# Kernel tuning notes

Measured on AMD Instinct MI355X. Metric: run time of the kernel, lower is better.

Reference implementation:

```python
import jax, jax.numpy as jnp
import numpy as np

N_NODES = 50000
N_EDGES = 800000
T = 3          # number of graph snapshots
L = 2          # num_layers
D = 128        # node feat dim == hidden dim
DE = 16        # edge feat dim


def setup_inputs() -> dict:
    key = jax.random.key(0)
    ks = jax.random.split(key, 12)
    return {
        "src": jax.random.randint(ks[0], (T, N_EDGES), 0, N_NODES, dtype=jnp.int32),
        "dst": jax.random.randint(ks[1], (T, N_EDGES), 0, N_NODES, dtype=jnp.int32),
        "n_feats": jax.random.normal(ks[2], (T, N_NODES, D), dtype=jnp.float32),
        "e_feats": jax.random.normal(ks[3], (T, N_EDGES, DE), dtype=jnp.float32),
        "W0": jax.random.normal(ks[4], (L, D, D), dtype=jnp.float32) * (1.0 / np.sqrt(D)),
        "lstm_Wih": jax.random.normal(ks[5], (L, 4 * D, D), dtype=jnp.float32) * (1.0 / np.sqrt(D)),
        "lstm_Whh": jax.random.normal(ks[6], (L, 4 * D, D), dtype=jnp.float32) * (1.0 / np.sqrt(D)),
        "lstm_bih": jnp.zeros((L, 4 * D), dtype=jnp.float32),
        "lstm_bhh": jnp.zeros((L, 4 * D), dtype=jnp.float32),
        "a_w": jax.random.normal(ks[7], (L, 2 * D + DE), dtype=jnp.float32) * 0.05,
    }


def _lstm(x, Wih, Whh, bih, bhh):
    # x: [S, H] unbatched sequence (S = D rows of W). PyTorch gate order i,f,g,o.
    H = Whh.shape[1]
    b = bih + bhh

    def step(carry, xt):
        h, c = carry
        gates = Wih @ xt + Whh @ h + b          # [4H]
        i = jax.nn.sigmoid(gates[:H])
        f = jax.nn.sigmoid(gates[H:2 * H])
        g = jnp.tanh(gates[2 * H:3 * H])
        o = jax.nn.sigmoid(gates[3 * H:])
        c = f * c + i * g
        h = o * jnp.tanh(c)
        return (h, c), h

    init = (jnp.zeros((H,), x.dtype), jnp.zeros((H,), x.dtype))
    _, hs = jax.lax.scan(step, init, x)
    return hs  # [S, H]


def _gat(src, dst, nf, ef, W, a_w, n_nodes):
    D_ = nf.shape[1]
    a_src, a_edge, a_dst = a_w[:D_], a_w[D_:D_ + ef.shape[1]], a_w[D_ + ef.shape[1]:]
    ft = nf @ W                                  # [N, H]
    s_src = nf @ a_src                           # [N]
    s_dst = nf @ a_dst                           # [N]
    score = s_src[src] + ef @ a_edge + s_dst[dst]  # [E]
    # edge softmax over destination neighborhoods
    mx = jax.ops.segment_max(score, dst, num_segments=n_nodes)
    ex = jnp.exp(score - mx[dst])
    den = jax.ops.segment_sum(ex, dst, num_segments=n_nodes)
    den = jnp.where(den == 0, 1.0, den)
    alpha = ex / den[dst]                        # [E]
    out = jax.ops.segment_sum(ft[src] * alpha[:, None], dst, num_segments=n_nodes)
    return jax.nn.leaky_relu(out)                # [N, H]


def reference(src, dst, n_feats, e_feats, W0, lstm_Wih, lstm_Whh, lstm_bih, lstm_bhh, a_w):
    n_nodes = n_feats.shape[1]
    feats = [n_feats[j] for j in range(n_feats.shape[0])]
    for i in range(W0.shape[0]):
        W = W0[i]
        for j in range(len(feats)):
            W = _lstm(W, lstm_Wih[i], lstm_Whh[i], lstm_bih[i], lstm_bhh[i])
            feats[j] = _gat(src[j], dst[j], feats[j], e_feats[j], W, a_w[i], n_nodes)
    return feats[-1]
```

## Files before the change

kernel.cpp:

```cpp
#include <hip/hip_runtime.h>
#include <cstdint>
#include <cstddef>

#define N_NODES 50000
#define N_EDGES 800000
#define D 128
#define DE 16
#define NBLK 196

typedef float v2f __attribute__((ext_vector_type(2)));

__global__ void csr_hist(const int* __restrict__ dst, int* __restrict__ count){
  int e = blockIdx.x*256 + threadIdx.x;
  if (e < N_EDGES) atomicAdd(&count[dst[e]], 1);
}

__global__ __launch_bounds__(256) void csr_blocksum(const int* __restrict__ count,
                                                    int* __restrict__ bsum){
  __shared__ int red[4];
  int i = blockIdx.x*256 + threadIdx.x;
  int v = (i < N_NODES) ? count[i] : 0;
  #pragma unroll
  for (int off=32; off; off>>=1) v += __shfl_down(v, off);
  if ((threadIdx.x & 63) == 0) red[threadIdx.x>>6] = v;
  __syncthreads();
  if (threadIdx.x == 0) bsum[blockIdx.x] = red[0]+red[1]+red[2]+red[3];
}

__global__ __launch_bounds__(256) void csr_scan_bsum(const int* __restrict__ bsum,
                                                     int* __restrict__ boff){
  __shared__ int s[256];
  int t = threadIdx.x;
  int v = (t < NBLK) ? bsum[t] : 0;
  s[t] = v; __syncthreads();
  for (int off=1; off<256; off<<=1){
    int u = (t >= off) ? s[t-off] : 0;
    __syncthreads(); s[t] += u; __syncthreads();
  }
  if (t < NBLK) boff[t] = s[t] - v;
}

__global__ __launch_bounds__(256) void csr_downsweep(const int* __restrict__ count,
    const int* __restrict__ boff, int* __restrict__ row_start, int* __restrict__ cursor){
  __shared__ int s[256];
  int t = threadIdx.x;
  int i = blockIdx.x*256 + t;
  int v = (i < N_NODES) ? count[i] : 0;
  s[t] = v; __syncthreads();
  for (int off=1; off<256; off<<=1){
    int u = (t >= off) ? s[t-off] : 0;
    __syncthreads(); s[t] += u; __syncthreads();
  }
  int excl = boff[blockIdx.x] + s[t] - v;
  if (i <= N_NODES) row_start[i] = excl;
  if (i <  N_NODES) cursor[i]   = excl;
}

__global__ void csr_scatter(const int* __restrict__ src, const int* __restrict__ dst,
                            int* __restrict__ cursor, int* __restrict__ perm,
                            int* __restrict__ src_perm){
  int e = blockIdx.x*256 + threadIdx.x;
  if (e >= N_EDGES) return;
  int d = dst[e];
  int pos = atomicAdd(&cursor[d], 1);
  perm[pos] = e;
  src_perm[pos] = src[e];
}

__global__ __launch_bounds__(512) void lstm_pre(const float* __restrict__ Wih,
     const float* __restrict__ bih, const float* __restrict__ bhh,
     const float* __restrict__ xin, float* __restrict__ P){
  __shared__ float xs[128];
  int i = blockIdx.x >> 7, t = blockIdx.x & 127;
  const float* x = xin + (size_t)i*16384;
  if (threadIdx.x < 128) xs[threadIdx.x] = x[t*128 + threadIdx.x];
  __syncthreads();
  int r = threadIdx.x;
  const float4* wr = (const float4*)(Wih + (size_t)(i*512 + r)*128);
  const float4* x4 = (const float4*)xs;
  float acc = bih[i*512+r] + bhh[i*512+r];
  #pragma unroll
  for (int k=0;k<32;k++){
    float4 w = wr[k]; float4 xv = x4[k];
    acc += w.x*xv.x + w.y*xv.y + w.z*xv.z + w.w*xv.w;
  }
  P[(size_t)(i*128+t)*512 + r] = acc;
}

__global__ __launch_bounds__(512, 2) void lstm_scan(const float* __restrict__ Whh,
     const float* __restrict__ P, float* __restrict__ xout){
  __shared__ float hs[128];
  __shared__ float part[4][512];
  const int i  = blockIdx.x;
  const int r  = threadIdx.x;
  const int w  = r >> 6;
  const int l  = r & 63;
  const int kc = w >> 1;
  const int rh = w & 1;
  const int row0 = rh*256 + l*4;
  v2f wv[4][16];
  {
    const float* base = Whh + (size_t)i*512*128 + (size_t)row0*128 + kc*32;
    #pragma unroll
    for (int ri=0; ri<4; ri++){
      const v2f* p2 = (const v2f*)(base + ri*128);
      #pragma unroll
      for (int j=0;j<16;j++) wv[ri][j] = p2[j];
    }
  }
  float c = 0.f;
  float hreg = 0.f;
  if (r < 128) hs[r] = 0.f;
  __syncthreads();
  const float* Pi = P + (size_t)i*128*512;
  float* xo = xout + (size_t)i*128*128;
  for (int t=0; t<128; t++){
    float p0=0.f, p1=0.f, p2=0.f, p3=0.f;
    if (r < 128){
      p0 = Pi[t*512 +   0 + r];
      p1 = Pi[t*512 + 128 + r];
      p2 = Pi[t*512 + 256 + r];
      p3 = Pi[t*512 + 384 + r];
    }
    float4 hbuf[8];
    {
      const float4* h4 = ((const float4*)hs) + kc*8;
      #pragma unroll
      for (int j=0;j<8;j++) hbuf[j] = h4[j];
    }
    const v2f* h2 = (const v2f*)hbuf;
    v2f a0 = (v2f)(0.f), a1 = (v2f)(0.f), a2 = (v2f)(0.f), a3 = (v2f)(0.f);
    #pragma unroll
    for (int j=0;j<16;j++){
      v2f hv = h2[j];
      a0 = __builtin_elementwise_fma(wv[0][j], hv, a0);
      a1 = __builtin_elementwise_fma(wv[1][j], hv, a1);
      a2 = __builtin_elementwise_fma(wv[2][j], hv, a2);
      a3 = __builtin_elementwise_fma(wv[3][j], hv, a3);
    }
    float4 pr;
    pr.x = a0.x + a0.y;
    pr.y = a1.x + a1.y;
    pr.z = a2.x + a2.y;
    pr.w = a3.x + a3.y;
    *(float4*)&part[kc][row0] = pr;
    __syncthreads();
    if (r < 128){
      int j = r;
      float s0 = ((part[0][      j] + part[1][      j]) + (part[2][      j] + part[3][      j])) + p0;
      float s1 = ((part[0][128 + j] + part[1][128 + j]) + (part[2][128 + j] + part[3][128 + j])) + p1;
      float s2 = ((part[0][256 + j] + part[1][256 + j]) + (part[2][256 + j] + part[3][256 + j])) + p2;
      float s3 = ((part[0][384 + j] + part[1][384 + j]) + (part[2][384 + j] + part[3][384 + j])) + p3;
      float gi = __builtin_amdgcn_rcpf(1.f + __expf(-s0));
      float gf = __builtin_amdgcn_rcpf(1.f + __expf(-s1));
      float xg = fminf(fmaxf(s2, -15.f), 15.f);
      float eg = __expf(2.f*xg);
      float gg = (eg - 1.f) * __builtin_amdgcn_rcpf(eg + 1.f);
      float go = __builtin_amdgcn_rcpf(1.f + __expf(-s3));
      c = gf*c + gi*gg;
      float xc = fminf(fmaxf(c, -15.f), 15.f);
      float e2 = __expf(2.f*xc);
      float th = (e2 - 1.f) * __builtin_amdgcn_rcpf(e2 + 1.f);
      hreg = go*th;
      hs[j] = hreg;
    }
    __syncthreads();
    if (r < 128) xo[t*128 + r] = hreg;
  }
}

__global__ __launch_bounds__(256) void gat_transform(const float* __restrict__ f,
    const float* __restrict__ W, const float* __restrict__ aw,
    float* __restrict__ ft, float* __restrict__ s_src){
  __shared__ float Ws[64*128];
  __shared__ float fs[128*36];
  int n0 = blockIdx.x * 32;
  {
    int n = threadIdx.x >> 3, kq = threadIdx.x & 7;
    int gn = n0 + n;
    #pragma unroll
    for (int p=0;p<4;p++){
      int k = kq*16 + p*4;
      float4 v = make_float4(0.f,0.f,0.f,0.f);
      if (gn < N_NODES) v = *(const float4*)(f + (size_t)gn*128 + k);
      fs[(k+0)*36+n] = v.x; fs[(k+1)*36+n] = v.y;
      fs[(k+2)*36+n] = v.z; fs[(k+3)*36+n] = v.w;
    }
  }
  int jg = threadIdx.x & 31, ng = threadIdx.x >> 5;
  v2f A00=(v2f)(0.f), A01=A00, A10=A00, A11=A00;
  v2f A20=A00, A21=A00, A30=A00, A31=A00;
  for (int kk=0; kk<128; kk+=64){
    __syncthreads();
    {
      const float4* W4 = (const float4*)(W + (size_t)kk*128);
      float4* Ws4w = (float4*)Ws;
      for (int idx = threadIdx.x; idx < 2048; idx += 256) Ws4w[idx] = W4[idx];
    }
    __syncthreads();
    const float4* Ws4 = (const float4*)Ws;
    #pragma unroll 4
    for (int k2=0;k2<64;k2++){
      float4 wvv = Ws4[k2*32 + jg];
      v2f wl; wl.x = wvv.x; wl.y = wvv.y;
      v2f wh; wh.x = wvv.z; wh.y = wvv.w;
      float4 fv = *(const float4*)&fs[(kk+k2)*36 + (ng<<2)];
      v2f f0 = (v2f)(fv.x), f1 = (v2f)(fv.y), f2 = (v2f)(fv.z), f3 = (v2f)(fv.w);
      A00 = __builtin_elementwise_fma(wl, f0, A00);
      A01 = __builtin_elementwise_fma(wh, f0, A01);
      A10 = __builtin_elementwise_fma(wl, f1, A10);
      A11 = __builtin_elementwise_fma(wh, f1, A11);
      A20 = __builtin_elementwise_fma(wl, f2, A20);
      A21 = __builtin_elementwise_fma(wh, f2, A21);
      A30 = __builtin_elementwise_fma(wl, f3, A30);
      A31 = __builtin_elementwise_fma(wh, f3, A31);
    }
  }
  int nb = n0 + (ng<<2);
  float4 o0; o0.x=A00.x; o0.y=A00.y; o0.z=A01.x; o0.w=A01.y;
  float4 o1; o1.x=A10.x; o1.y=A10.y; o1.z=A11.x; o1.w=A11.y;
  float4 o2; o2.x=A20.x; o2.y=A20.y; o2.z=A21.x; o2.w=A21.y;
  float4 o3; o3.x=A30.x; o3.y=A30.y; o3.z=A31.x; o3.w=A31.y;
  if (nb+0 < N_NODES) *(float4*)(ft + (size_t)(nb+0)*128 + (jg<<2)) = o0;
  if (nb+1 < N_NODES) *(float4*)(ft + (size_t)(nb+1)*128 + (jg<<2)) = o1;
  if (nb+2 < N_NODES) *(float4*)(ft + (size_t)(nb+2)*128 + (jg<<2)) = o2;
  if (nb+3 < N_NODES) *(float4*)(ft + (size_t)(nb+3)*128 + (jg<<2)) = o3;
  if (threadIdx.x < 32){
    int gn = n0 + threadIdx.x;
    if (gn < N_NODES){
      float s = 0.f;
      for (int k=0;k<128;k++) s += fs[k*36 + threadIdx.x] * aw[k];
      s_src[gn] = s;
    }
  }
}

__global__ __launch_bounds__(256) void gat_edge_score(const int* __restrict__ perm,
    const int* __restrict__ src_perm, const float* __restrict__ s_src,
    const float* __restrict__ ef, const float* __restrict__ aw,
    float* __restrict__ score){
  int p = blockIdx.x*256 + threadIdx.x;
  if (p >= N_EDGES) return;
  int e = perm[p];
  int s = src_perm[p];
  const float4* A = (const float4*)(aw + 128);
  float4 A0=A[0], A1=A[1], A2=A[2], A3=A[3];
  const float4* ev = (const float4*)(ef + (size_t)e*16);
  float4 v0=ev[0], v1=ev[1], v2=ev[2], v3=ev[3];
  float acc = s_src[s];
  acc += v0.x*A0.x + v0.y*A0.y + v0.z*A0.z + v0.w*A0.w;
  acc += v1.x*A1.x + v1.y*A1.y + v1.z*A1.z + v1.w*A1.w;
  acc += v2.x*A2.x + v2.y*A2.y + v2.z*A2.z + v2.w*A2.w;
  acc += v3.x*A3.x + v3.y*A3.y + v3.z*A3.z + v3.w*A3.w;
  score[p] = acc;
}

__global__ __launch_bounds__(256) void gat_aggregate(const int* __restrict__ row_start,
    const int* __restrict__ src_perm, float* __restrict__ score,
    const float* __restrict__ ft, float* __restrict__ out){
  int lane = threadIdx.x & 63;
  int wv = threadIdx.x >> 6;
  int n = blockIdx.x*4 + wv;
  if (n >= N_NODES) return;
  int s = row_start[n], e = row_start[n+1];
  float m = -1e30f;
  for (int p = s+lane; p < e; p += 64) m = fmaxf(m, score[p]);
  #pragma unroll
  for (int off=32; off; off>>=1) m = fmaxf(m, __shfl_xor(m, off));
  float den = 0.f;
  for (int p = s+lane; p < e; p += 64){
    float ex = __expf(score[p]-m);
    den += ex;
    score[p] = ex;
  }
  #pragma unroll
  for (int off=32; off; off>>=1) den += __shfl_xor(den, off);
  float inv = (den > 0.f) ? 1.f/den : 0.f;
  float a0 = 0.f, a1 = 0.f;
  for (int p = s; p < e; p++){
    float al = score[p]*inv;
    int sp = src_perm[p];
    float2 v = ((const float2*)(ft + (size_t)sp*128))[lane];
    a0 += al*v.x; a1 += al*v.y;
  }
  float2 o;
  o.x = (a0 > 0.f) ? a0 : 0.01f*a0;
  o.y = (a1 > 0.f) ? a1 : 0.01f*a1;
  ((float2*)(out + (size_t)n*128))[lane] = o;
}

extern "C" void kernel_launch(void* const* d_in, const int* in_sizes, int n_in,
                              void* d_out, int out_size, void* d_ws, size_t ws_size,
                              hipStream_t stream){
  (void)in_sizes; (void)n_in; (void)out_size; (void)ws_size;
  const int*   src     = (const int*)d_in[0] + (size_t)2*N_EDGES;
  const int*   dst     = (const int*)d_in[1] + (size_t)2*N_EDGES;
  const float* n_feats = (const float*)d_in[2] + (size_t)2*N_NODES*D;
  const float* e_feats = (const float*)d_in[3] + (size_t)2*N_EDGES*DE;
  const float* W0      = (const float*)d_in[4];
  const float* Wih     = (const float*)d_in[5];
  const float* Whh     = (const float*)d_in[6];
  const float* bih     = (const float*)d_in[7];
  const float* bhh     = (const float*)d_in[8];
  const float* a_w     = (const float*)d_in[9];
  float* out = (float*)d_out;

  char* wsp = (char*)d_ws;
  auto alloc = [&](size_t bytes)->char*{
    char* p = wsp; wsp += (bytes + 255) & ~(size_t)255; return p;
  };
  float* P         = (float*)alloc((size_t)2*128*512*4);
  float* xA        = (float*)alloc((size_t)2*128*128*4);
  float* xB        = (float*)alloc((size_t)2*128*128*4);
  int*   count     = (int*)  alloc((size_t)N_NODES*4);
  int*   bsum      = (int*)  alloc((size_t)NBLK*4);
  int*   boff      = (int*)  alloc((size_t)NBLK*4);
  int*   row_start = (int*)  alloc((size_t)(N_NODES+1)*4);
  int*   cursor    = (int*)  alloc((size_t)N_NODES*4);
  int*   perm      = (int*)  alloc((size_t)N_EDGES*4);
  int*   src_perm  = (int*)  alloc((size_t)N_EDGES*4);
  float* score     = (float*)alloc((size_t)N_EDGES*4);
  float* s_src     = (float*)alloc((size_t)N_NODES*4);
  float* ft        = (float*)alloc((size_t)N_NODES*D*4);
  float* f1        = (float*)alloc((size_t)N_NODES*D*4);

  hipMemsetAsync(count, 0, (size_t)N_NODES*4, stream);
  csr_hist     <<<(N_EDGES+255)/256, 256, 0, stream>>>(dst, count);
  csr_blocksum <<<NBLK, 256, 0, stream>>>(count, bsum);
  csr_scan_bsum<<<1,    256, 0, stream>>>(bsum, boff);
  csr_downsweep<<<NBLK, 256, 0, stream>>>(count, boff, row_start, cursor);
  csr_scatter  <<<(N_EDGES+255)/256, 256, 0, stream>>>(src, dst, cursor, perm, src_perm);

  const float* xi = W0;
  float* xo = xA;
  for (int app=0; app<3; app++){
    lstm_pre <<<256, 512, 0, stream>>>(Wih, bih, bhh, xi, P);
    lstm_scan<<<2,   512, 0, stream>>>(Whh, P, xo);
    xi = xo;
    xo = (app==0) ? xB : xA;
  }
  const float* Wfin = xA;

  const float* fin = n_feats;
  for (int l=0; l<2; l++){
    float* outl = (l==0) ? f1 : out;
    gat_transform <<<(N_NODES+31)/32, 256, 0, stream>>>(fin, Wfin + (size_t)l*16384,
                                                        a_w + (size_t)l*272, ft, s_src);
    gat_edge_score<<<(N_EDGES+255)/256, 256, 0, stream>>>(perm, src_perm, s_src,
                                                          e_feats, a_w + (size_t)l*272, score);
    gat_aggregate <<<N_NODES/4, 256, 0, stream>>>(row_start, src_perm, score, ft, outl);
    fin = f1;
  }
}
```

Measured before the change: 930.5 us.

## Fuse three chained LSTM scans into one wavefront-pipelined kernel

Replaces the three sequential lstm_pre + lstm_scan launches with one precompute launch and a single fused kernel. That kernel runs the three LSTM applications as a diagonal wavefront: at step d, stage a processes timestep d-a, and stages 2 and 3 compute their input projection on the fly from the previous stage's hidden state using register-resident Wih. This removes two of the three serial 128-step latency chains and four kernel launches. In exchange it doubles register use for weights (launch bounds drop to 1 block per SM) and adds extra FMA work and shared-memory traffic to each step.

Result: slower. 1.841 ms (+97.8%).

```diff
diff --git a/kernel.cpp b/kernel.cpp
--- a/kernel.cpp
+++ b/kernel.cpp
@@ -87,10 +87,13 @@
   P[(size_t)(i*128+t)*512 + r] = acc;
 }
 
-__global__ __launch_bounds__(512, 2) void lstm_scan(const float* __restrict__ Whh,
-     const float* __restrict__ P, float* __restrict__ xout){
-  __shared__ float hs[128];
-  __shared__ float part[4][512];
+__global__ __launch_bounds__(512, 1) void lstm_fused(
+    const float* __restrict__ Whh, const float* __restrict__ Wih,
+    const float* __restrict__ bih, const float* __restrict__ bhh,
+    const float* __restrict__ P0, float* __restrict__ xout){
+  __shared__ float hs[3][128];
+  __shared__ float partW[3][4][512];
+  __shared__ float partP[2][4][512];
   const int i  = blockIdx.x;
   const int r  = threadIdx.x;
   const int w  = r >> 6;
@@ -98,59 +101,101 @@
   const int kc = w >> 1;
   const int rh = w & 1;
   const int row0 = rh*256 + l*4;
-  v2f wv[4][16];
+  v2f whh[4][16], wih[4][16];
   {
-    const float* base = Whh + (size_t)i*512*128 + (size_t)row0*128 + kc*32;
+    const float* bh = Whh + (size_t)i*65536 + (size_t)row0*128 + kc*32;
+    const float* bw = Wih + (size_t)i*65536 + (size_t)row0*128 + kc*32;
     #pragma unroll
     for (int ri=0; ri<4; ri++){
-      const v2f* p2 = (const v2f*)(base + ri*128);
+      const v2f* ph = (const v2f*)(bh + ri*128);
+      const v2f* pw = (const v2f*)(bw + ri*128);
       #pragma unroll
-      for (int j=0;j<16;j++) wv[ri][j] = p2[j];
-    }
+      for (int j=0;j<16;j++){ whh[ri][j] = ph[j]; wih[ri][j] = pw[j]; }
+    }
+  }
+  const int sa = r >> 7;
+  const int sj = r & 127;
+  float b0=0.f,b1=0.f,b2=0.f,b3=0.f;
+  if (sa==1 || sa==2){
+    b0 = bih[i*512 +       sj] + bhh[i*512 +       sj];
+    b1 = bih[i*512 + 128 + sj] + bhh[i*512 + 128 + sj];
+    b2 = bih[i*512 + 256 + sj] + bhh[i*512 + 256 + sj];
+    b3 = bih[i*512 + 384 + sj] + bhh[i*512 + 384 + sj];
   }
   float c = 0.f;
   float hreg = 0.f;
-  if (r < 128) hs[r] = 0.f;
+  if (r < 384) ((float*)hs)[r] = 0.f;
   __syncthreads();
-  const float* Pi = P + (size_t)i*128*512;
+  const float* Pi = P0 + (size_t)i*128*512;
   float* xo = xout + (size_t)i*128*128;
-  for (int t=0; t<128; t++){
-    float p0=0.f, p1=0.f, p2=0.f, p3=0.f;
-    if (r < 128){
-      p0 = Pi[t*512 +   0 + r];
-      p1 = Pi[t*512 + 128 + r];
-      p2 = Pi[t*512 + 256 + r];
-      p3 = Pi[t*512 + 384 + r];
-    }
-    float4 hbuf[8];
-    {
-      const float4* h4 = ((const float4*)hs) + kc*8;
-      #pragma unroll
-      for (int j=0;j<8;j++) hbuf[j] = h4[j];
-    }
-    const v2f* h2 = (const v2f*)hbuf;
-    v2f a0 = (v2f)(0.f), a1 = (v2f)(0.f), a2 = (v2f)(0.f), a3 = (v2f)(0.f);
+  for (int d=0; d<130; d++){
+    float pc0=0.f,pc1=0.f,pc2=0.f,pc3=0.f;
+    if (sa==0 && d<128){
+      pc0 = Pi[d*512 +       sj];
+      pc1 = Pi[d*512 + 128 + sj];
+      pc2 = Pi[d*512 + 256 + sj];
+      pc3 = Pi[d*512 + 384 + sj];
+    }
     #pragma unroll
-    for (int j=0;j<16;j++){
-      v2f hv = h2[j];
-      a0 = __builtin_elementwise_fma(wv[0][j], hv, a0);
-      a1 = __builtin_elementwise_fma(wv[1][j], hv, a1);
-      a2 = __builtin_elementwise_fma(wv[2][j], hv, a2);
-      a3 = __builtin_elementwise_fma(wv[3][j], hv, a3);
-    }
-    float4 pr;
-    pr.x = a0.x + a0.y;
-    pr.y = a1.x + a1.y;
-    pr.z = a2.x + a2.y;
-    pr.w = a3.x + a3.y;
-    *(float4*)&part[kc][row0] = pr;
+    for (int a=0; a<3; a++){
+      const int ta = d - a;
+      const bool rec  = (ta >= 0) && (ta < 128);
+      const bool feed = (a < 2) && (ta >= 1) && (ta <= 128);
+      if (rec || feed){
+        float4 hb[8];
+        const float4* h4 = ((const float4*)hs[a]) + kc*8;
+        #pragma unroll
+        for (int j=0;j<8;j++) hb[j] = h4[j];
+        const v2f* h2 = (const v2f*)hb;
+        if (rec){
+          v2f a0=(v2f)(0.f), a1=a0, a2=a0, a3=a0;
+          #pragma unroll
+          for (int j=0;j<16;j++){
+            v2f hv = h2[j];
+            a0 = __builtin_elementwise_fma(whh[0][j], hv, a0);
+            a1 = __builtin_elementwise_fma(whh[1][j], hv, a1);
+            a2 = __builtin_elementwise_fma(whh[2][j], hv, a2);
+            a3 = __builtin_elementwise_fma(whh[3][j], hv, a3);
+          }
+          float4 pr;
+          pr.x = a0.x + a0.y; pr.y = a1.x + a1.y;
+          pr.z = a2.x + a2.y; pr.w = a3.x + a3.y;
+          *(float4*)&partW[a][kc][row0] = pr;
+        }
+        if (feed){
+          v2f a0=(v2f)(0.f), a1=a0, a2=a0, a3=a0;
+          #pragma unroll
+          for (int j=0;j<16;j++){
+            v2f hv = h2[j];
+            a0 = __builtin_elementwise_fma(wih[0][j], hv, a0);
+            a1 = __builtin_elementwise_fma(wih[1][j], hv, a1);
+            a2 = __builtin_elementwise_fma(wih[2][j], hv, a2);
+            a3 = __builtin_elementwise_fma(wih[3][j], hv, a3);
+          }
+          float4 pr;
+          pr.x = a0.x + a0.y; pr.y = a1.x + a1.y;
+          pr.z = a2.x + a2.y; pr.w = a3.x + a3.y;
+          *(float4*)&partP[a][kc][row0] = pr;
+        }
+      }
+    }
     __syncthreads();
-    if (r < 128){
-      int j = r;
-      float s0 = ((part[0][      j] + part[1][      j]) + (part[2][      j] + part[3][      j])) + p0;
-      float s1 = ((part[0][128 + j] + part[1][128 + j]) + (part[2][128 + j] + part[3][128 + j])) + p1;
-      float s2 = ((part[0][256 + j] + part[1][256 + j]) + (part[2][256 + j] + part[3][256 + j])) + p2;
-      float s3 = ((part[0][384 + j] + part[1][384 + j]) + (part[2][384 + j] + part[3][384 + j])) + p3;
+    const int ts = d - sa;
+    if (sa < 3 && ts >= 0 && ts < 128){
+      const int j0 = sj, j1 = 128+sj, j2 = 256+sj, j3 = 384+sj;
+      float s0 = (partW[sa][0][j0]+partW[sa][1][j0])+(partW[sa][2][j0]+partW[sa][3][j0]);
+      float s1 = (partW[sa][0][j1]+partW[sa][1][j1])+(partW[sa][2][j1]+partW[sa][3][j1]);
+      float s2 = (partW[sa][0][j2]+partW[sa][1][j2])+(partW[sa][2][j2]+partW[sa][3][j2]);
+      float s3 = (partW[sa][0][j3]+partW[sa][1][j3])+(partW[sa][2][j3]+partW[sa][3][j3]);
+      if (sa == 0){
+        s0 += pc0; s1 += pc1; s2 += pc2; s3 += pc3;
+      } else {
+        const float (*pp)[512] = partP[sa-1];
+        s0 += ((pp[0][j0]+pp[1][j0])+(pp[2][j0]+pp[3][j0])) + b0;
+        s1 += ((pp[0][j1]+pp[1][j1])+(pp[2][j1]+pp[3][j1])) + b1;
+        s2 += ((pp[0][j2]+pp[1][j2])+(pp[2][j2]+pp[3][j2])) + b2;
+        s3 += ((pp[0][j3]+pp[1][j3])+(pp[2][j3]+pp[3][j3])) + b3;
+      }
       float gi = __builtin_amdgcn_rcpf(1.f + __expf(-s0));
       float gf = __builtin_amdgcn_rcpf(1.f + __expf(-s1));
       float xg = fminf(fmaxf(s2, -15.f), 15.f);
@@ -162,10 +207,10 @@
       float e2 = __expf(2.f*xc);
       float th = (e2 - 1.f) * __builtin_amdgcn_rcpf(e2 + 1.f);
       hreg = go*th;
-      hs[j] = hreg;
+      hs[sa][sj] = hreg;
     }
     __syncthreads();
-    if (r < 128) xo[t*128 + r] = hreg;
+    if (sa == 2 && ts >= 0 && ts < 128) xo[ts*128 + sj] = hreg;
   }
 }
 
@@ -310,8 +355,7 @@
     char* p = wsp; wsp += (bytes + 255) & ~(size_t)255; return p;
   };
   float* P         = (float*)alloc((size_t)2*128*512*4);
-  float* xA        = (float*)alloc((size_t)2*128*128*4);
-  float* xB        = (float*)alloc((size_t)2*128*128*4);
+  float* Wfin      = (float*)alloc((size_t)2*128*128*4);
   int*   count     = (int*)  alloc((size_t)N_NODES*4);
   int*   bsum      = (int*)  alloc((size_t)NBLK*4);
   int*   boff      = (int*)  alloc((size_t)NBLK*4);
@@ -331,15 +375,8 @@
   csr_downsweep<<<NBLK, 256, 0, stream>>>(count, boff, row_start, cursor);
   csr_scatter  <<<(N_EDGES+255)/256, 256, 0, stream>>>(src, dst, cursor, perm, src_perm);
 
-  const float* xi = W0;
-  float* xo = xA;
-  for (int app=0; app<3; app++){
-    lstm_pre <<<256, 512, 0, stream>>>(Wih, bih, bhh, xi, P);
-    lstm_scan<<<2,   512, 0, stream>>>(Whh, P, xo);
-    xi = xo;
-    xo = (app==0) ? xB : xA;
-  }
-  const float* Wfin = xA;
+  lstm_pre  <<<256, 512, 0, stream>>>(Wih, bih, bhh, W0, P);
+  lstm_fused<<<2,   512, 0, stream>>>(Whh, Wih, bih, bhh, P, Wfin);
 
   const float* fin = n_feats;
   for (int l=0; l<2; l++){
```

## Co-schedule CSR build and edge-score precompute inside LSTM scan kernels

Applied to the files above, without the earlier changes.

The separate CSR-construction kernels are folded into the LSTM pre/scan launches as extra blocks, so the serial 2-block LSTM scan overlaps with the histogram, prefix sums and scatter. The edge-feature dot products for both layers are computed once in unpermuted order alongside the first scan. The edge-score kernel then only gathers precomputed values. This removes launches and idle GPU time during the latency-bound scan. In exchange it adds an 800K x 2 float buffer and a random gather via perm.

New measurement: 838.3 us. 9.9% less time.

```diff
diff --git a/kernel.cpp b/kernel.cpp
--- a/kernel.cpp
+++ b/kernel.cpp
@@ -6,72 +6,17 @@
 #define N_EDGES 800000
 #define D 128
 #define DE 16
-#define NBLK 196
+#define HB 1563
+#define NB512 98
 
 typedef float v2f __attribute__((ext_vector_type(2)));
 
-__global__ void csr_hist(const int* __restrict__ dst, int* __restrict__ count){
-  int e = blockIdx.x*256 + threadIdx.x;
-  if (e < N_EDGES) atomicAdd(&count[dst[e]], 1);
-}
-
-__global__ __launch_bounds__(256) void csr_blocksum(const int* __restrict__ count,
-                                                    int* __restrict__ bsum){
-  __shared__ int red[4];
-  int i = blockIdx.x*256 + threadIdx.x;
-  int v = (i < N_NODES) ? count[i] : 0;
-  #pragma unroll
-  for (int off=32; off; off>>=1) v += __shfl_down(v, off);
-  if ((threadIdx.x & 63) == 0) red[threadIdx.x>>6] = v;
-  __syncthreads();
-  if (threadIdx.x == 0) bsum[blockIdx.x] = red[0]+red[1]+red[2]+red[3];
-}
-
-__global__ __launch_bounds__(256) void csr_scan_bsum(const int* __restrict__ bsum,
-                                                     int* __restrict__ boff){
-  __shared__ int s[256];
-  int t = threadIdx.x;
-  int v = (t < NBLK) ? bsum[t] : 0;
-  s[t] = v; __syncthreads();
-  for (int off=1; off<256; off<<=1){
-    int u = (t >= off) ? s[t-off] : 0;
-    __syncthreads(); s[t] += u; __syncthreads();
-  }
-  if (t < NBLK) boff[t] = s[t] - v;
-}
-
-__global__ __launch_bounds__(256) void csr_downsweep(const int* __restrict__ count,
-    const int* __restrict__ boff, int* __restrict__ row_start, int* __restrict__ cursor){
-  __shared__ int s[256];
-  int t = threadIdx.x;
-  int i = blockIdx.x*256 + t;
-  int v = (i < N_NODES) ? count[i] : 0;
-  s[t] = v; __syncthreads();
-  for (int off=1; off<256; off<<=1){
-    int u = (t >= off) ? s[t-off] : 0;
-    __syncthreads(); s[t] += u; __syncthreads();
-  }
-  int excl = boff[blockIdx.x] + s[t] - v;
-  if (i <= N_NODES) row_start[i] = excl;
-  if (i <  N_NODES) cursor[i]   = excl;
-}
-
-__global__ void csr_scatter(const int* __restrict__ src, const int* __restrict__ dst,
-                            int* __restrict__ cursor, int* __restrict__ perm,
-                            int* __restrict__ src_perm){
-  int e = blockIdx.x*256 + threadIdx.x;
-  if (e >= N_EDGES) return;
-  int d = dst[e];
-  int pos = atomicAdd(&cursor[d], 1);
-  perm[pos] = e;
-  src_perm[pos] = src[e];
-}
-
-__global__ __launch_bounds__(512) void lstm_pre(const float* __restrict__ Wih,
+
+__device__ void lstm_pre_body(const float* __restrict__ Wih,
      const float* __restrict__ bih, const float* __restrict__ bhh,
-     const float* __restrict__ xin, float* __restrict__ P){
+     const float* __restrict__ xin, float* __restrict__ P, int bid){
   __shared__ float xs[128];
-  int i = blockIdx.x >> 7, t = blockIdx.x & 127;
+  int i = bid >> 7, t = bid & 127;
   const float* x = xin + (size_t)i*16384;
   if (threadIdx.x < 128) xs[threadIdx.x] = x[t*128 + threadIdx.x];
   __syncthreads();
@@ -87,11 +32,10 @@
   P[(size_t)(i*128+t)*512 + r] = acc;
 }
 
-__global__ __launch_bounds__(512, 2) void lstm_scan(const float* __restrict__ Whh,
-     const float* __restrict__ P, float* __restrict__ xout){
+__device__ void lstm_scan_body(const float* __restrict__ Whh,
+     const float* __restrict__ P, float* __restrict__ xout, int i){
   __shared__ float hs[128];
   __shared__ float part[4][512];
-  const int i  = blockIdx.x;
   const int r  = threadIdx.x;
   const int w  = r >> 6;
   const int l  = r & 63;
@@ -169,6 +113,131 @@
   }
 }
 
+__device__ void csr_blocksum512(const int* __restrict__ count,
+                                int* __restrict__ bsum, int b){
+  __shared__ int red[8];
+  int t = threadIdx.x;
+  int i = b*512 + t;
+  int v = (i < N_NODES) ? count[i] : 0;
+  #pragma unroll
+  for (int off=32; off; off>>=1) v += __shfl_down(v, off);
+  if ((t & 63) == 0) red[t>>6] = v;
+  __syncthreads();
+  if (t == 0){
+    int s = 0;
+    #pragma unroll
+    for (int k=0;k<8;k++) s += red[k];
+    bsum[b] = s;
+  }
+}
+
+__device__ void csr_scan_bsum512(const int* __restrict__ bsum,
+                                 int* __restrict__ boff){
+  __shared__ int s[512];
+  int t = threadIdx.x;
+  int v = (t < NB512) ? bsum[t] : 0;
+  s[t] = v; __syncthreads();
+  for (int off=1; off<512; off<<=1){
+    int u = (t >= off) ? s[t-off] : 0;
+    __syncthreads(); s[t] += u; __syncthreads();
+  }
+  if (t < NB512) boff[t] = s[t] - v;
+}
+
+__device__ void csr_downsweep512(const int* __restrict__ count,
+    const int* __restrict__ boff, int* __restrict__ row_start,
+    int* __restrict__ cursor, int b){
+  __shared__ int s[512];
+  int t = threadIdx.x;
+  int i = b*512 + t;
+  int v = (i < N_NODES) ? count[i] : 0;
+  s[t] = v; __syncthreads();
+  for (int off=1; off<512; off<<=1){
+    int u = (t >= off) ? s[t-off] : 0;
+    __syncthreads(); s[t] += u; __syncthreads();
+  }
+  int excl = boff[b] + s[t] - v;
+  if (i <= N_NODES) row_start[i] = excl;
+  if (i <  N_NODES) cursor[i]   = excl;
+}
+
+__global__ __launch_bounds__(512) void k_pre(const float* __restrict__ Wih,
+     const float* __restrict__ bih, const float* __restrict__ bhh,
+     const float* __restrict__ xin, float* __restrict__ P){
+  lstm_pre_body(Wih, bih, bhh, xin, P, blockIdx.x);
+}
+
+__global__ __launch_bounds__(512, 2) void k_scan_hist_epart(
+    const float* __restrict__ Whh, const float* __restrict__ P,
+    float* __restrict__ xout, const int* __restrict__ dst,
+    int* __restrict__ count, const float* __restrict__ ef,
+    const float* __restrict__ aw, float* __restrict__ epart){
+  int b = blockIdx.x;
+  if (b < 2){ lstm_scan_body(Whh, P, xout, b); return; }
+  b -= 2;
+  if (b < HB){
+    int e = b*512 + threadIdx.x;
+    if (e < N_EDGES) atomicAdd(&count[dst[e]], 1);
+    return;
+  }
+  b -= HB;
+  int e = b*512 + threadIdx.x;
+  if (e < N_EDGES){
+    const float4* ev = (const float4*)(ef + (size_t)e*16);
+    float4 v0=ev[0], v1=ev[1], v2=ev[2], v3=ev[3];
+    #pragma unroll
+    for (int l=0; l<2; l++){
+      const float4* A = (const float4*)(aw + l*272 + 128);
+      float4 A0=A[0], A1=A[1], A2=A[2], A3=A[3];
+      float acc = v0.x*A0.x + v0.y*A0.y + v0.z*A0.z + v0.w*A0.w;
+      acc      += v1.x*A1.x + v1.y*A1.y + v1.z*A1.z + v1.w*A1.w;
+      acc      += v2.x*A2.x + v2.y*A2.y + v2.z*A2.z + v2.w*A2.w;
+      acc      += v3.x*A3.x + v3.y*A3.y + v3.z*A3.z + v3.w*A3.w;
+      epart[(size_t)l*N_EDGES + e] = acc;
+    }
+  }
+}
+
+__global__ __launch_bounds__(512) void k_pre_blocksum(const float* __restrict__ Wih,
+     const float* __restrict__ bih, const float* __restrict__ bhh,
+     const float* __restrict__ xin, float* __restrict__ P,
+     const int* __restrict__ count, int* __restrict__ bsum){
+  if (blockIdx.x < 256) lstm_pre_body(Wih, bih, bhh, xin, P, blockIdx.x);
+  else                  csr_blocksum512(count, bsum, blockIdx.x - 256);
+}
+
+__global__ __launch_bounds__(512, 2) void k_scan_scanbsum(
+    const float* __restrict__ Whh, const float* __restrict__ P,
+    float* __restrict__ xout, const int* __restrict__ bsum,
+    int* __restrict__ boff){
+  if (blockIdx.x < 2) lstm_scan_body(Whh, P, xout, blockIdx.x);
+  else                csr_scan_bsum512(bsum, boff);
+}
+
+__global__ __launch_bounds__(512) void k_pre_downsweep(const float* __restrict__ Wih,
+     const float* __restrict__ bih, const float* __restrict__ bhh,
+     const float* __restrict__ xin, float* __restrict__ P,
+     const int* __restrict__ count, const int* __restrict__ boff,
+     int* __restrict__ row_start, int* __restrict__ cursor){
+  if (blockIdx.x < 256) lstm_pre_body(Wih, bih, bhh, xin, P, blockIdx.x);
+  else                  csr_downsweep512(count, boff, row_start, cursor, blockIdx.x - 256);
+}
+
+__global__ __launch_bounds__(512, 2) void k_scan_scatter(
+    const float* __restrict__ Whh, const float* __restrict__ P,
+    float* __restrict__ xout, const int* __restrict__ src,
+    const int* __restrict__ dst, int* __restrict__ cursor,
+    int* __restrict__ perm, int* __restrict__ src_perm){
+  int b = blockIdx.x;
+  if (b < 2){ lstm_scan_body(Whh, P, xout, b); return; }
+  int e = (b-2)*512 + threadIdx.x;
+  if (e >= N_EDGES) return;
+  int d = dst[e];
+  int pos = atomicAdd(&cursor[d], 1);
+  perm[pos] = e;
+  src_perm[pos] = src[e];
+}
+
 __global__ __launch_bounds__(256) void gat_transform(const float* __restrict__ f,
     const float* __restrict__ W, const float* __restrict__ aw,
     float* __restrict__ ft, float* __restrict__ s_src){
@@ -237,22 +306,10 @@
 
 __global__ __launch_bounds__(256) void gat_edge_score(const int* __restrict__ perm,
     const int* __restrict__ src_perm, const float* __restrict__ s_src,
-    const float* __restrict__ ef, const float* __restrict__ aw,
-    float* __restrict__ score){
+    const float* __restrict__ epart_l, float* __restrict__ score){
   int p = blockIdx.x*256 + threadIdx.x;
   if (p >= N_EDGES) return;
-  int e = perm[p];
-  int s = src_perm[p];
-  const float4* A = (const float4*)(aw + 128);
-  float4 A0=A[0], A1=A[1], A2=A[2], A3=A[3];
-  const float4* ev = (const float4*)(ef + (size_t)e*16);
-  float4 v0=ev[0], v1=ev[1], v2=ev[2], v3=ev[3];
-  float acc = s_src[s];
-  acc += v0.x*A0.x + v0.y*A0.y + v0.z*A0.z + v0.w*A0.w;
-  acc += v1.x*A1.x + v1.y*A1.y + v1.z*A1.z + v1.w*A1.w;
-  acc += v2.x*A2.x + v2.y*A2.y + v2.z*A2.z + v2.w*A2.w;
-  acc += v3.x*A3.x + v3.y*A3.y + v3.z*A3.z + v3.w*A3.w;
-  score[p] = acc;
+  score[p] = s_src[src_perm[p]] + epart_l[perm[p]];
 }
 
 __global__ __launch_bounds__(256) void gat_aggregate(const int* __restrict__ row_start,
@@ -313,32 +370,30 @@
   float* xA        = (float*)alloc((size_t)2*128*128*4);
   float* xB        = (float*)alloc((size_t)2*128*128*4);
   int*   count     = (int*)  alloc((size_t)N_NODES*4);
-  int*   bsum      = (int*)  alloc((size_t)NBLK*4);
-  int*   boff      = (int*)  alloc((size_t)NBLK*4);
+  int*   bsum      = (int*)  alloc((size_t)NB512*4);
+  int*   boff      = (int*)  alloc((size_t)NB512*4);
   int*   row_start = (int*)  alloc((size_t)(N_NODES+1)*4);
   int*   cursor    = (int*)  alloc((size_t)N_NODES*4);
   int*   perm      = (int*)  alloc((size_t)N_EDGES*4);
   int*   src_perm  = (int*)  alloc((size_t)N_EDGES*4);
   float* score     = (float*)alloc((size_t)N_EDGES*4);
   float* s_src     = (float*)alloc((size_t)N_NODES*4);
+  float* epart     = (float*)alloc((size_t)2*N_EDGES*4);
   float* ft        = (float*)alloc((size_t)N_NODES*D*4);
   float* f1        = (float*)alloc((size_t)N_NODES*D*4);
 
   hipMemsetAsync(count, 0, (size_t)N_NODES*4, stream);
-  csr_hist     <<<(N_EDGES+255)/256, 256, 0, stream>>>(dst, count);
-  csr_blocksum <<<NBLK, 256, 0, stream>>>(count, bsum);
-  csr_scan_bsum<<<1,    256, 0, stream>>>(bsum, boff);
-  csr_downsweep<<<NBLK, 256, 0, stream>>>(count, boff, row_start, cursor);
-  csr_scatter  <<<(N_EDGES+255)/256, 256, 0, stream>>>(src, dst, cursor, perm, src_perm);
-
-  const float* xi = W0;
-  float* xo = xA;
-  for (int app=0; app<3; app++){
-    lstm_pre <<<256, 512, 0, stream>>>(Wih, bih, bhh, xi, P);
-    lstm_scan<<<2,   512, 0, stream>>>(Whh, P, xo);
-    xi = xo;
-    xo = (app==0) ? xB : xA;
-  }
+
+  k_pre            <<<256,        512, 0, stream>>>(Wih, bih, bhh, W0, P);
+  k_scan_hist_epart<<<2 + 2*HB,   512, 0, stream>>>(Whh, P, xA, dst, count,
+                                                    e_feats, a_w, epart);
+  k_pre_blocksum   <<<256 + NB512,512, 0, stream>>>(Wih, bih, bhh, xA, P,
+                                                    count, bsum);
+  k_scan_scanbsum  <<<3,          512, 0, stream>>>(Whh, P, xB, bsum, boff);
+  k_pre_downsweep  <<<256 + NB512,512, 0, stream>>>(Wih, bih, bhh, xB, P,
+                                                    count, boff, row_start, cursor);
+  k_scan_scatter   <<<2 + HB,     512, 0, stream>>>(Whh, P, xA, src, dst,
+                                                    cursor, perm, src_perm);
   const float* Wfin = xA;
 
   const float* fin = n_feats;
@@ -347,7 +402,7 @@
     gat_transform <<<(N_NODES+31)/32, 256, 0, stream>>>(fin, Wfin + (size_t)l*16384,
                                                         a_w + (size_t)l*272, ft, s_src);
     gat_edge_score<<<(N_EDGES+255)/256, 256, 0, stream>>>(perm, src_perm, s_src,
-                                                          e_feats, a_w + (size_t)l*272, score);
+                                                          epart + (size_t)l*N_EDGES, score);
     gat_aggregate <<<N_NODES/4, 256, 0, stream>>>(row_start, src_perm, score, ft, outl);
     fin = f1;
   }
```
